# Optimization experiments

Measured on AMD Instinct MI355X. Metric: run time of the kernel, lower is better.

## Reference

```python
import jax, jax.numpy as jnp
import numpy as np

LEAF = 32
N = 262144          # num_nodes, power of 2
NLEV = 8            # HODLR levels
RANK = 16           # off-diagonal low-rank
NNZ = 1310720       # ~5 nnz per row


def setup_inputs() -> dict:
    key = jax.random.key(0)
    ks = jax.random.split(key, 24)
    inp = {}
    inp["leaf_blocks"] = jax.random.normal(ks[0], (1, N // LEAF, LEAF, LEAF), jnp.float32) * 0.1
    for l in range(NLEV):
        inp[f"u{l}"] = jax.random.normal(ks[1 + 2 * l], (1, N, RANK), jnp.float32) * 0.05
        inp[f"v{l}"] = jax.random.normal(ks[2 + 2 * l], (1, N, RANK), jnp.float32) * 0.05
    inp["A_indices"] = jax.random.randint(ks[17], (2, NNZ), 0, N, dtype=jnp.int32).astype(jnp.int64)
    inp["A_values"] = jax.random.normal(ks[18], (NNZ,), jnp.float32)
    inp["z"] = jax.random.normal(ks[19], (1, N, 1), jnp.float32)
    inp["num_nodes"] = N
    return inp


def apply_hodlr(leaf_blocks, factors, x, leaf_size=LEAF):
    # x: [B, n, 1]; leaf_blocks: [B, n/leaf, leaf, leaf]
    B, n, _ = x.shape
    nb = n // leaf_size
    xb = x.reshape(B, nb, leaf_size, 1)
    L = leaf_blocks
    # y = L @ (L^T @ x) + 1e-4 * x  per leaf block
    yb = jnp.matmul(L, jnp.matmul(jnp.swapaxes(L, -1, -2), xb)) + xb * 1e-4
    y = yb.reshape(B, n, 1)
    for li, (u, v) in enumerate(factors):
        num_splits = 2 ** (li + 1)
        bs = n // num_splits
        if bs == 0:
            continue
        npair = num_splits // 2
        vl = npair * 2 * bs  # == n for power-of-2 n
        xv = x[:, :vl].reshape(B, npair, 2, bs, 1)
        uv = u[:, :vl].reshape(B, npair, 2, bs, -1)
        vv = v[:, :vl].reshape(B, npair, 2, bs, -1)
        xL, xR = xv[:, :, 0], xv[:, :, 1]
        uL, uR = uv[:, :, 0], uv[:, :, 1]
        vL, vR = vv[:, :, 0], vv[:, :, 1]
        # cross-block low-rank updates: y_L += U_L (V_R^T x_R), y_R += U_R (V_L^T x_L)
        yL = jnp.matmul(uL, jnp.matmul(jnp.swapaxes(vR, -1, -2), xR))
        yR = jnp.matmul(uR, jnp.matmul(jnp.swapaxes(vL, -1, -2), xL))
        upd = jnp.stack([yL, yR], axis=2).reshape(B, vl, 1)
        if vl < n:
            upd = jnp.pad(upd, ((0, 0), (0, n - vl), (0, 0)))
        y = y + upd
    return y


def reference(leaf_blocks, u0, v0, u1, v1, u2, v2, u3, v3, u4, v4, u5, v5, u6, v6, u7, v7,
              A_indices, A_values, z, num_nodes):
    factors = [(u0, v0), (u1, v1), (u2, v2), (u3, v3),
               (u4, v4), (u5, v5), (u6, v6), (u7, v7)]
    w = apply_hodlr(leaf_blocks, factors, z)           # [1, N, 1]
    w_flat = w[0, :, 0]                                 # [N]
    rows, cols = A_indices[0], A_indices[1]
    # sparse COO matvec: y[r] = sum_k A_values[k] * w[cols[k]] over rows
    y_flat = jax.ops.segment_sum(A_values * w_flat[cols], rows, num_segments=num_nodes)
    y = y_flat.reshape(1, num_nodes, 1)
    return jnp.mean((y - z) ** 2)
```

## Files before the change

### kernel.cpp

```cpp
#include <hip/hip_runtime.h>

#define NN 262144
#define RANK 16
#define NNZ_K 1310720
#define NCH 2048

struct P8 { const float* p[8]; };

__global__ __launch_bounds__(256, 6) void k_levels_t(P8 v, const float* __restrict__ z,
                                                     float* __restrict__ part) {
    __shared__ float red[8][4][16];
    const int tid  = threadIdx.x;
    const int base = blockIdx.x * 128;
    const int q    = tid & 3;
    const int e    = tid >> 2;
    const int lane = tid & 63;
    const int wv   = tid >> 6;

#pragma unroll
    for (int g = 0; g < 2; ++g) {
        float4 acc[4];
#pragma unroll
        for (int l = 0; l < 4; ++l) acc[l] = make_float4(0.f, 0.f, 0.f, 0.f);

#pragma unroll
        for (int it = 0; it < 2; ++it) {
            const int jl = it * 64 + e;
            const size_t j = (size_t)(base + jl);
            const float zz = z[j];
            float4 vv[4];
#pragma unroll
            for (int l = 0; l < 4; ++l)
                vv[l] = *(const float4*)(v.p[g * 4 + l] + j * RANK + q * 4);
#pragma unroll
            for (int l = 0; l < 4; ++l) {
                acc[l].x += vv[l].x * zz;
                acc[l].y += vv[l].y * zz;
                acc[l].z += vv[l].z * zz;
                acc[l].w += vv[l].w * zz;
            }
        }

#pragma unroll
        for (int l = 0; l < 4; ++l) {
            float4 a = acc[l];
#pragma unroll
            for (int m = 4; m <= 32; m <<= 1) {
                a.x += __shfl_xor(a.x, m);
                a.y += __shfl_xor(a.y, m);
                a.z += __shfl_xor(a.z, m);
                a.w += __shfl_xor(a.w, m);
            }
            if (lane < 4) *(float4*)&red[g * 4 + l][wv][lane * 4] = a;
        }
    }
    __syncthreads();

    if (tid < 128) {
        const int l = tid >> 4;
        const int r = tid & 15;
        const float s = red[l][0][r] + red[l][1][r] + red[l][2][r] + red[l][3][r];
        part[(l * NCH + blockIdx.x) * 16 + r] = s;
    }
}

__global__ __launch_bounds__(256) void k_reduce_t(const float* __restrict__ part,
                                                  float* __restrict__ tg,
                                                  float* __restrict__ loss) {
    const int b = blockIdx.x;
    if (b == 0 && threadIdx.x == 0) loss[0] = 0.f;
    const int t = b + 2;
    const int l = 30 - __clz(t);
    const int h = t - (2 << l);
    const int cnt = 1024 >> l;
    const int c0  = h * cnt;
    const int r = threadIdx.x & 15;
    const int g = threadIdx.x >> 4;

    float s = 0.f;
    for (int c = c0 + g; c < c0 + cnt; c += 16)
        s += part[(l * NCH + c) * 16 + r];

    __shared__ float red[256];
    red[threadIdx.x] = s;
    __syncthreads();
    if (threadIdx.x < 16) {
        float ss = 0.f;
#pragma unroll
        for (int k = 0; k < 16; ++k) ss += red[k * 16 + r];
        tg[((2 << l) - 2 + h) * 16 + r] = ss;
    }
}

__global__ __launch_bounds__(256, 6) void k_w(const float* __restrict__ leaf, P8 u,
                                              const float* __restrict__ z,
                                              const float* __restrict__ tg,
                                              float* __restrict__ w,
                                              float* __restrict__ y) {
    __shared__ float wl[128];
    __shared__ float pb[128];
    __shared__ float tl[8][16];

    const int tid  = threadIdx.x;
    const int base = blockIdx.x * 128;

    if (tid < 128) {
        const int l = tid >> 4;
        const int r = tid & 15;
        const int h = base >> (17 - l);
        tl[l][r] = tg[(((2 << l) - 2) + (h ^ 1)) * 16 + r];
    }

    {
        const int l6 = tid & 63;
        const int wv = tid >> 6;
        const int b  = blockIdx.x * 4 + wv;
        const int r  = l6 >> 1;

        const float* Lb = leaf + (size_t)b * 1024 + r * 32 + (l6 & 1) * 16;
        const float4 L0 = ((const float4*)Lb)[0];
        const float4 L1 = ((const float4*)Lb)[1];
        const float4 L2 = ((const float4*)Lb)[2];
        const float4 L3 = ((const float4*)Lb)[3];

        const float zl = z[b * 32 + (l6 & 31)];
        const float xr = __shfl(zl, r);

        float4 t0 = make_float4(L0.x * xr, L0.y * xr, L0.z * xr, L0.w * xr);
        float4 t1 = make_float4(L1.x * xr, L1.y * xr, L1.z * xr, L1.w * xr);
        float4 t2 = make_float4(L2.x * xr, L2.y * xr, L2.z * xr, L2.w * xr);
        float4 t3 = make_float4(L3.x * xr, L3.y * xr, L3.z * xr, L3.w * xr);

#pragma unroll
        for (int m = 2; m <= 32; m <<= 1) {
            t0.x += __shfl_xor(t0.x, m); t0.y += __shfl_xor(t0.y, m);
            t0.z += __shfl_xor(t0.z, m); t0.w += __shfl_xor(t0.w, m);
            t1.x += __shfl_xor(t1.x, m); t1.y += __shfl_xor(t1.y, m);
            t1.z += __shfl_xor(t1.z, m); t1.w += __shfl_xor(t1.w, m);
            t2.x += __shfl_xor(t2.x, m); t2.y += __shfl_xor(t2.y, m);
            t2.z += __shfl_xor(t2.z, m); t2.w += __shfl_xor(t2.w, m);
            t3.x += __shfl_xor(t3.x, m); t3.y += __shfl_xor(t3.y, m);
            t3.z += __shfl_xor(t3.z, m); t3.w += __shfl_xor(t3.w, m);
        }

        float yp = L0.x * t0.x + L0.y * t0.y + L0.z * t0.z + L0.w * t0.w
                 + L1.x * t1.x + L1.y * t1.y + L1.z * t1.z + L1.w * t1.w
                 + L2.x * t2.x + L2.y * t2.y + L2.z * t2.z + L2.w * t2.w
                 + L3.x * t3.x + L3.y * t3.y + L3.z * t3.z + L3.w * t3.w;
        yp += __shfl_xor(yp, 1);

        const float w0  = yp + 1e-4f * xr;
        const float out = __shfl(w0, (l6 & 31) * 2);
        if (l6 < 32) wl[wv * 32 + l6] = out;
    }
    __syncthreads();

    const int half = tid >> 7;
    const int e    = tid & 127;
    const size_t i = (size_t)(base + e);
    const int l0   = half * 4;

    float accs[4];
#pragma unroll
    for (int lp = 0; lp < 2; ++lp) {
        const int l = l0 + lp * 2;
        float4 a[8];
        {
            const float4* up0 = (const float4*)(u.p[l] + i * RANK);
            const float4* up1 = (const float4*)(u.p[l + 1] + i * RANK);
#pragma unroll
            for (int k = 0; k < 4; ++k) a[k]     = up0[k];
#pragma unroll
            for (int k = 0; k < 4; ++k) a[4 + k] = up1[k];
        }
#pragma unroll
        for (int s = 0; s < 2; ++s) {
            const float4 t0 = *(const float4*)&tl[l + s][0];
            const float4 t1 = *(const float4*)&tl[l + s][4];
            const float4 t2 = *(const float4*)&tl[l + s][8];
            const float4 t3 = *(const float4*)&tl[l + s][12];
            const float4* av = &a[s * 4];
            accs[lp * 2 + s] = av[0].x * t0.x + av[0].y * t0.y + av[0].z * t0.z + av[0].w * t0.w
                             + av[1].x * t1.x + av[1].y * t1.y + av[1].z * t1.z + av[1].w * t1.w
                             + av[2].x * t2.x + av[2].y * t2.y + av[2].z * t2.z + av[2].w * t2.w
                             + av[3].x * t3.x + av[3].y * t3.y + av[3].z * t3.z + av[3].w * t3.w;
        }
    }
    const float sum = (accs[0] + accs[1]) + (accs[2] + accs[3]);
    if (half) pb[e] = sum;
    __syncthreads();
    if (!half) {
        w[i] = wl[e] + sum + pb[e];
        y[i] = 0.f;
    }
}

__global__ __launch_bounds__(256) void k_spmv(const int* __restrict__ idx,
                                              const float* __restrict__ vals,
                                              const float* __restrict__ w,
                                              float* __restrict__ y) {
    const int k = (blockIdx.x * 256 + threadIdx.x) * 4;
    const int4   r4 = *(const int4*)(idx + k);
    const int4   c4 = *(const int4*)(idx + NNZ_K + k);
    const float4 v4 = *(const float4*)(vals + k);
    atomicAdd(&y[r4.x], v4.x * w[c4.x]);
    atomicAdd(&y[r4.y], v4.y * w[c4.y]);
    atomicAdd(&y[r4.z], v4.z * w[c4.z]);
    atomicAdd(&y[r4.w], v4.w * w[c4.w]);
}

__global__ __launch_bounds__(256) void k_loss(const float* __restrict__ y,
                                              const float* __restrict__ z,
                                              float* __restrict__ loss) {
    const int i = blockIdx.x * 256 + threadIdx.x;
    const float4 a = ((const float4*)y)[i];
    const float4 b = ((const float4*)z)[i];
    const float dx = a.x - b.x, dy = a.y - b.y, dz = a.z - b.z, dw = a.w - b.w;
    float s = dx * dx + dy * dy + dz * dz + dw * dw;
#pragma unroll
    for (int m = 32; m >= 1; m >>= 1) s += __shfl_down(s, m);
    __shared__ float r4s[4];
    const int lane = threadIdx.x & 63, wv = threadIdx.x >> 6;
    if (lane == 0) r4s[wv] = s;
    __syncthreads();
    if (threadIdx.x == 0) atomicAdd(loss, r4s[0] + r4s[1] + r4s[2] + r4s[3]);
}

__global__ void k_fin(const float* __restrict__ loss, float* __restrict__ out) {
    out[0] = loss[0] * (1.0f / (float)NN);
}

extern "C" void kernel_launch(void* const* d_in, const int* in_sizes, int n_in,
                              void* d_out, int out_size, void* d_ws, size_t ws_size,
                              hipStream_t stream) {
    const float* leaf = (const float*)d_in[0];
    P8 u, v;
    for (int l = 0; l < 8; ++l) {
        u.p[l] = (const float*)d_in[1 + 2 * l];
        v.p[l] = (const float*)d_in[2 + 2 * l];
    }
    const int*   Aidx  = (const int*)d_in[17];
    const float* Avals = (const float*)d_in[18];
    const float* z     = (const float*)d_in[19];

    float* ws   = (float*)d_ws;
    float* part = ws;
    float* tg   = ws + 262144;
    float* loss = ws + 270336;
    float* w    = ws + 270400;
    float* y    = ws + 532544;

    k_levels_t<<<NCH, 256, 0, stream>>>(v, z, part);
    k_reduce_t<<<510, 256, 0, stream>>>(part, tg, loss);
    k_w       <<<NN / 128, 256, 0, stream>>>(leaf, u, z, tg, w, y);
    k_spmv    <<<NNZ_K / 1024, 256, 0, stream>>>(Aidx, Avals, w, y);
    k_loss    <<<NN / 1024, 256, 0, stream>>>(y, z, loss);
    k_fin     <<<1, 1, 0, stream>>>(loss, (float*)d_out);
}
```

Before: 404.5 us.

## Fuse all stages into one cooperative persistent kernel with grid syncs

Replaces the six separate kernel launches (level projections, tree reduction, HODLR apply, SpMV, loss, finalize) with a single cooperative kernel of 1024 blocks that loops over chunks and separates stages with grid.sync(). The aim is to remove per-launch overhead and the gaps between dependent kernels. In exchange it adds grid-wide barriers and fewer concurrent blocks per stage, and it falls back to the old launches if the cooperative launch fails.

Measured after the change: 1.479 ms. +265.7%, slower.

```diff
diff --git a/kernel.cpp b/kernel.cpp
--- a/kernel.cpp
+++ b/kernel.cpp
@@ -1,11 +1,248 @@
 #include <hip/hip_runtime.h>
+#include <hip/hip_cooperative_groups.h>
+
+namespace cg = cooperative_groups;
 
 #define NN 262144
 #define RANK 16
 #define NNZ_K 1310720
 #define NCH 2048
+#define GRID 1024
 
 struct P8 { const float* p[8]; };
+
+__global__ __launch_bounds__(256, 4) void k_all(const float* __restrict__ leaf,
+                                                P8 u, P8 v,
+                                                const int* __restrict__ idx,
+                                                const float* __restrict__ vals,
+                                                const float* __restrict__ z,
+                                                float* __restrict__ part,
+                                                float* __restrict__ tg,
+                                                float* __restrict__ loss,
+                                                float* __restrict__ w,
+                                                float* __restrict__ y,
+                                                float* __restrict__ out) {
+    cg::grid_group grid = cg::this_grid();
+    const int tid = threadIdx.x;
+    const int bid = blockIdx.x;
+
+    __shared__ float red[8][4][16];
+    __shared__ float red2[256];
+    __shared__ float wl[128];
+    __shared__ float pb[128];
+    __shared__ float tl[8][16];
+    __shared__ float rl[4];
+
+    y[bid * 256 + tid] = 0.f;
+    if (bid == 0 && tid == 0) loss[0] = 0.f;
+
+    {
+        const int q    = tid & 3;
+        const int e    = tid >> 2;
+        const int lane = tid & 63;
+        const int wv   = tid >> 6;
+
+        for (int ch = bid; ch < NCH; ch += GRID) {
+            const int base = ch * 128;
+#pragma unroll
+            for (int g = 0; g < 2; ++g) {
+                float4 acc[4];
+#pragma unroll
+                for (int l = 0; l < 4; ++l) acc[l] = make_float4(0.f, 0.f, 0.f, 0.f);
+#pragma unroll
+                for (int it = 0; it < 2; ++it) {
+                    const int jl = it * 64 + e;
+                    const size_t j = (size_t)(base + jl);
+                    const float zz = z[j];
+                    float4 vv[4];
+#pragma unroll
+                    for (int l = 0; l < 4; ++l)
+                        vv[l] = *(const float4*)(v.p[g * 4 + l] + j * RANK + q * 4);
+#pragma unroll
+                    for (int l = 0; l < 4; ++l) {
+                        acc[l].x += vv[l].x * zz;
+                        acc[l].y += vv[l].y * zz;
+                        acc[l].z += vv[l].z * zz;
+                        acc[l].w += vv[l].w * zz;
+                    }
+                }
+#pragma unroll
+                for (int l = 0; l < 4; ++l) {
+                    float4 a = acc[l];
+#pragma unroll
+                    for (int m = 4; m <= 32; m <<= 1) {
+                        a.x += __shfl_xor(a.x, m);
+                        a.y += __shfl_xor(a.y, m);
+                        a.z += __shfl_xor(a.z, m);
+                        a.w += __shfl_xor(a.w, m);
+                    }
+                    if (lane < 4) *(float4*)&red[g * 4 + l][wv][lane * 4] = a;
+                }
+            }
+            __syncthreads();
+            if (tid < 128) {
+                const int l = tid >> 4;
+                const int r = tid & 15;
+                const float s = red[l][0][r] + red[l][1][r] + red[l][2][r] + red[l][3][r];
+                part[(l * NCH + ch) * 16 + r] = s;
+            }
+            __syncthreads();
+        }
+    }
+    __threadfence();
+    grid.sync();
+
+    if (bid < 510) {
+        const int t = bid + 2;
+        const int l = 30 - __clz(t);
+        const int h = t - (2 << l);
+        const int cnt = 1024 >> l;
+        const int c0  = h * cnt;
+        const int r = tid & 15;
+        const int g = tid >> 4;
+
+        float s = 0.f;
+        for (int c = c0 + g; c < c0 + cnt; c += 16)
+            s += part[(l * NCH + c) * 16 + r];
+
+        red2[tid] = s;
+        __syncthreads();
+        if (tid < 16) {
+            float ss = 0.f;
+#pragma unroll
+            for (int k = 0; k < 16; ++k) ss += red2[k * 16 + r];
+            tg[((2 << l) - 2 + h) * 16 + r] = ss;
+        }
+    }
+    __threadfence();
+    grid.sync();
+
+    for (int ch = bid; ch < NCH; ch += GRID) {
+        const int base = ch * 128;
+
+        if (tid < 128) {
+            const int l = tid >> 4;
+            const int r = tid & 15;
+            const int h = base >> (17 - l);
+            tl[l][r] = tg[(((2 << l) - 2) + (h ^ 1)) * 16 + r];
+        }
+
+        {
+            const int l6 = tid & 63;
+            const int wv = tid >> 6;
+            const int b  = ch * 4 + wv;
+            const int r  = l6 >> 1;
+
+            const float* Lb = leaf + (size_t)b * 1024 + r * 32 + (l6 & 1) * 16;
+            const float4 L0 = ((const float4*)Lb)[0];
+            const float4 L1 = ((const float4*)Lb)[1];
+            const float4 L2 = ((const float4*)Lb)[2];
+            const float4 L3 = ((const float4*)Lb)[3];
+
+            const float zl = z[b * 32 + (l6 & 31)];
+            const float xr = __shfl(zl, r);
+
+            float4 t0 = make_float4(L0.x * xr, L0.y * xr, L0.z * xr, L0.w * xr);
+            float4 t1 = make_float4(L1.x * xr, L1.y * xr, L1.z * xr, L1.w * xr);
+            float4 t2 = make_float4(L2.x * xr, L2.y * xr, L2.z * xr, L2.w * xr);
+            float4 t3 = make_float4(L3.x * xr, L3.y * xr, L3.z * xr, L3.w * xr);
+
+#pragma unroll
+            for (int m = 2; m <= 32; m <<= 1) {
+                t0.x += __shfl_xor(t0.x, m); t0.y += __shfl_xor(t0.y, m);
+                t0.z += __shfl_xor(t0.z, m); t0.w += __shfl_xor(t0.w, m);
+                t1.x += __shfl_xor(t1.x, m); t1.y += __shfl_xor(t1.y, m);
+                t1.z += __shfl_xor(t1.z, m); t1.w += __shfl_xor(t1.w, m);
+                t2.x += __shfl_xor(t2.x, m); t2.y += __shfl_xor(t2.y, m);
+                t2.z += __shfl_xor(t2.z, m); t2.w += __shfl_xor(t2.w, m);
+                t3.x += __shfl_xor(t3.x, m); t3.y += __shfl_xor(t3.y, m);
+                t3.z += __shfl_xor(t3.z, m); t3.w += __shfl_xor(t3.w, m);
+            }
+
+            float yp = L0.x * t0.x + L0.y * t0.y + L0.z * t0.z + L0.w * t0.w
+                     + L1.x * t1.x + L1.y * t1.y + L1.z * t1.z + L1.w * t1.w
+                     + L2.x * t2.x + L2.y * t2.y + L2.z * t2.z + L2.w * t2.w
+                     + L3.x * t3.x + L3.y * t3.y + L3.z * t3.z + L3.w * t3.w;
+            yp += __shfl_xor(yp, 1);
+
+            const float w0  = yp + 1e-4f * xr;
+            const float o   = __shfl(w0, (l6 & 31) * 2);
+            if (l6 < 32) wl[wv * 32 + l6] = o;
+        }
+        __syncthreads();
+
+        {
+            const int half = tid >> 7;
+            const int e    = tid & 127;
+            const size_t i = (size_t)(base + e);
+            const int l0   = half * 4;
+
+            float accs[4];
+#pragma unroll
+            for (int lp = 0; lp < 2; ++lp) {
+                const int l = l0 + lp * 2;
+                float4 a[8];
+                {
+                    const float4* up0 = (const float4*)(u.p[l] + i * RANK);
+                    const float4* up1 = (const float4*)(u.p[l + 1] + i * RANK);
+#pragma unroll
+                    for (int k = 0; k < 4; ++k) a[k]     = up0[k];
+#pragma unroll
+                    for (int k = 0; k < 4; ++k) a[4 + k] = up1[k];
+                }
+#pragma unroll
+                for (int s = 0; s < 2; ++s) {
+                    const float4 t0 = *(const float4*)&tl[l + s][0];
+                    const float4 t1 = *(const float4*)&tl[l + s][4];
+                    const float4 t2 = *(const float4*)&tl[l + s][8];
+                    const float4 t3 = *(const float4*)&tl[l + s][12];
+                    const float4* av = &a[s * 4];
+                    accs[lp * 2 + s] = av[0].x * t0.x + av[0].y * t0.y + av[0].z * t0.z + av[0].w * t0.w
+                                     + av[1].x * t1.x + av[1].y * t1.y + av[1].z * t1.z + av[1].w * t1.w
+                                     + av[2].x * t2.x + av[2].y * t2.y + av[2].z * t2.z + av[2].w * t2.w
+                                     + av[3].x * t3.x + av[3].y * t3.y + av[3].z * t3.z + av[3].w * t3.w;
+                }
+            }
+            const float sum = (accs[0] + accs[1]) + (accs[2] + accs[3]);
+            if (half) pb[e] = sum;
+            __syncthreads();
+            if (!half) w[i] = wl[e] + sum + pb[e];
+        }
+        __syncthreads();
+    }
+    __threadfence();
+    grid.sync();
+
+    {
+        const int id = bid * 256 + tid;
+        for (int k = id * 4; k < NNZ_K; k += GRID * 256 * 4) {
+            const int4   r4 = *(const int4*)(idx + k);
+            const int4   c4 = *(const int4*)(idx + NNZ_K + k);
+            const float4 v4 = *(const float4*)(vals + k);
+            atomicAdd(&y[r4.x], v4.x * w[c4.x]);
+            atomicAdd(&y[r4.y], v4.y * w[c4.y]);
+            atomicAdd(&y[r4.z], v4.z * w[c4.z]);
+            atomicAdd(&y[r4.w], v4.w * w[c4.w]);
+        }
+    }
+    __threadfence();
+    grid.sync();
+
+    {
+        const int id = bid * 256 + tid;
+        const float d = y[id] - z[id];
+        float s = d * d;
+#pragma unroll
+        for (int m = 32; m >= 1; m >>= 1) s += __shfl_down(s, m);
+        if ((tid & 63) == 0) rl[tid >> 6] = s;
+        __syncthreads();
+        if (tid == 0) atomicAdd(loss, rl[0] + rl[1] + rl[2] + rl[3]);
+    }
+    __threadfence();
+    grid.sync();
+
+    if (bid == 0 && tid == 0) out[0] = loss[0] * (1.0f / (float)NN);
+}
 
 __global__ __launch_bounds__(256, 6) void k_levels_t(P8 v, const float* __restrict__ z,
                                                      float* __restrict__ part) {
@@ -22,7 +259,6 @@
         float4 acc[4];
 #pragma unroll
         for (int l = 0; l < 4; ++l) acc[l] = make_float4(0.f, 0.f, 0.f, 0.f);
-
 #pragma unroll
         for (int it = 0; it < 2; ++it) {
             const int jl = it * 64 + e;
@@ -40,7 +276,6 @@
                 acc[l].w += vv[l].w * zz;
             }
         }
-
 #pragma unroll
         for (int l = 0; l < 4; ++l) {
             float4 a = acc[l];
@@ -249,11 +484,20 @@
     float* loss = ws + 270336;
     float* w    = ws + 270400;
     float* y    = ws + 532544;
-
-    k_levels_t<<<NCH, 256, 0, stream>>>(v, z, part);
-    k_reduce_t<<<510, 256, 0, stream>>>(part, tg, loss);
-    k_w       <<<NN / 128, 256, 0, stream>>>(leaf, u, z, tg, w, y);
-    k_spmv    <<<NNZ_K / 1024, 256, 0, stream>>>(Aidx, Avals, w, y);
-    k_loss    <<<NN / 1024, 256, 0, stream>>>(y, z, loss);
-    k_fin     <<<1, 1, 0, stream>>>(loss, (float*)d_out);
-}
+    float* outp = (float*)d_out;
+
+    void* args[] = { (void*)&leaf, (void*)&u, (void*)&v, (void*)&Aidx,
+                     (void*)&Avals, (void*)&z, (void*)&part, (void*)&tg,
+                     (void*)&loss, (void*)&w, (void*)&y, (void*)&outp };
+
+    hipError_t err = hipLaunchCooperativeKernel((const void*)k_all, dim3(GRID),
+                                                dim3(256), args, 0, stream);
+    if (err != hipSuccess) {
+        k_levels_t<<<NCH, 256, 0, stream>>>(v, z, part);
+        k_reduce_t<<<510, 256, 0, stream>>>(part, tg, loss);
+        k_w       <<<NN / 128, 256, 0, stream>>>(leaf, u, z, tg, w, y);
+        k_spmv    <<<NNZ_K / 1024, 256, 0, stream>>>(Aidx, Avals, w, y);
+        k_loss    <<<NN / 1024, 256, 0, stream>>>(y, z, loss);
+        k_fin     <<<1, 1, 0, stream>>>(loss, outp);
+    }
+}
```
